# Kernel tuning notes

Hardware: AMD Instinct MI355X
Metric: run time of the kernel (lower is better)

## Reference

```python
import jax, jax.numpy as jnp
import numpy as np

CLASS_NUM = 20
C_FEAT = 256
STRIDE = 16
ROI = 7
SCALE = 1.0 / 16.0
TOPK = 300
NMS_THR = 0.7
SCORE_THR = 0.5
SAMPLES = 2  # nearest samples per bin edge in roi_pool


def _conv(x, W, b, stride, padding):
    y = jax.lax.conv_general_dilated(x, W, (stride, stride), padding,
                                     dimension_numbers=('NCHW', 'OIHW', 'NCHW'))
    return y + b[None, :, None, None]


def _pairwise_iou(boxes):
    x1, y1, x2, y2 = boxes[:, 0], boxes[:, 1], boxes[:, 2], boxes[:, 3]
    area = jnp.maximum(x2 - x1, 0.) * jnp.maximum(y2 - y1, 0.)
    ix1 = jnp.maximum(x1[:, None], x1[None, :])
    iy1 = jnp.maximum(y1[:, None], y1[None, :])
    ix2 = jnp.minimum(x2[:, None], x2[None, :])
    iy2 = jnp.minimum(y2[:, None], y2[None, :])
    inter = jnp.maximum(ix2 - ix1, 0.) * jnp.maximum(iy2 - iy1, 0.)
    return inter / jnp.maximum(area[:, None] + area[None, :] - inter, 1e-6)


def _nms(boxes, scores, valid, thr):
    # fixed-size greedy NMS: returns boolean keep mask aligned with input order
    K = boxes.shape[0]
    order = jnp.argsort(-scores)
    b = boxes[order]
    v = valid[order]
    iou = _pairwise_iou(b)  # [K,K]
    idx = jnp.arange(K)

    def body(i, keep):
        k = keep[i] & v[i]
        suppress = (iou[i] > thr) & (idx > i) & k
        return keep & (~suppress)

    keep = jax.lax.fori_loop(0, K, body, v)
    return jnp.zeros((K,), bool).at[order].set(keep)


def _roi_pool(f, boxes):
    # f: [C,H,W] feature map; boxes: [K,4] in image coords.
    # Max pool over ROI x SAMPLES nearest-neighbor samples per bin (jit-safe roi_pool).
    C, H, W = f.shape
    K = boxes.shape[0]
    b = boxes * SCALE
    frac = (jnp.arange(ROI)[:, None] + (jnp.arange(SAMPLES)[None, :] + 0.5) / SAMPLES).reshape(-1) / ROI
    xs = b[:, 0:1] + frac[None, :] * (b[:, 2:3] - b[:, 0:1])  # [K, ROI*S]
    ys = b[:, 1:2] + frac[None, :] * (b[:, 3:4] - b[:, 1:2])
    ix = jnp.clip(jnp.floor(xs), 0, W - 1).astype(jnp.int32)
    iy = jnp.clip(jnp.floor(ys), 0, H - 1).astype(jnp.int32)
    g = f[:, iy[:, :, None], ix[:, None, :]]  # [C,K,ROI*S,ROI*S]
    g = g.reshape(C, K, ROI, SAMPLES, ROI, SAMPLES)
    return g.max(axis=(3, 5)).transpose(1, 0, 2, 3)  # [K,C,ROI,ROI]


def setup_inputs() -> dict:
    key = jax.random.key(0)
    ks = jax.random.split(key, 12)
    img = 800
    x = jax.random.uniform(ks[0], (1, 3, img, img), jnp.float32)
    gt_boxes = jax.random.uniform(ks[1], (8, 5), jnp.float32) * img

    def w_(k, shape, fan_in):
        return jax.random.normal(k, shape, jnp.float32) * (1.0 / np.sqrt(fan_in))

    d_flat = ROI * ROI * C_FEAT
    return {
        'x': x, 'gt_boxes': gt_boxes,
        'W_feat': w_(ks[2], (C_FEAT, 3, STRIDE, STRIDE), 3 * STRIDE * STRIDE),
        'b_feat': jnp.zeros((C_FEAT,), jnp.float32),
        'W1': w_(ks[3], (C_FEAT, C_FEAT, 3, 3), C_FEAT * 9),
        'b1': jnp.zeros((C_FEAT,), jnp.float32),
        'Wc': w_(ks[4], (2, C_FEAT), C_FEAT),
        'bc': jnp.zeros((2,), jnp.float32),
        'Wb': w_(ks[5], (4, C_FEAT), C_FEAT),
        'bb': jnp.zeros((4,), jnp.float32),
        'fc1_w': w_(ks[6], (4096, d_flat), d_flat),
        'fc1_b': jnp.zeros((4096,), jnp.float32),
        'fc2_w': w_(ks[7], (4096, 4096), 4096),
        'fc2_b': jnp.zeros((4096,), jnp.float32),
        'cls_w': w_(ks[8], (CLASS_NUM + 1, 4096), 4096),
        'cls_b': jnp.zeros((CLASS_NUM + 1,), jnp.float32),
        'box_w': w_(ks[9], (4, 4096), 4096),
        'box_b': jnp.zeros((4,), jnp.float32),
        'w': 800, 'h': 800,
    }


def reference(x, gt_boxes, W_feat, b_feat, W1, b1, Wc, bc, Wb, bb,
              fc1_w, fc1_b, fc2_w, fc2_b, cls_w, cls_b, box_w, box_b, w, h):
    feature = _conv(x, W_feat, b_feat, STRIDE, 'VALID')          # [1,C,50,50]
    hmap = jax.nn.relu(_conv(feature, W1, b1, 1, 'SAME'))
    pre_labels = (jnp.einsum('nchw,oc->nhwo', hmap, Wc) + bc).reshape(-1, 2)
    pre_boxes = (jnp.einsum('nchw,oc->nhwo', hmap, Wb) + bb).reshape(-1, 4)
    logits = jax.nn.softmax(pre_labels, axis=-1)[:, 1]           # [2500]
    scores, idx = jax.lax.top_k(logits, TOPK)                    # fixed-size stand-in for score>thr select
    valid = scores > SCORE_THR
    pb = pre_boxes[idx]
    wf = jnp.float32(w)
    hf = jnp.float32(h)
    # box decode exactly as the original per-box loop (vectorized)
    x1 = jnp.maximum(pb[:, 2] - pb[:, 0] / 2, 0.)
    y1 = jnp.maximum(pb[:, 3] - pb[:, 1] / 2, 0.)
    x2 = jnp.minimum(pb[:, 2] + pb[:, 0], wf)
    y2 = jnp.minimum(pb[:, 3] + pb[:, 1], hf)
    boxes = jnp.stack([x1, y1, x2, y2], axis=-1)                 # [K,4]
    keep = _nms(boxes, scores, valid, NMS_THR)
    pooled = _roi_pool(feature[0], boxes)                        # [K,C,7,7]
    flat = pooled.reshape(TOPK, -1)
    h1 = jax.nn.relu(flat @ fc1_w.T + fc1_b)
    h2 = jax.nn.relu(h1 @ fc2_w.T + fc2_b)
    cls = h2 @ cls_w.T + cls_b                                   # [K,21]
    box = h2 @ box_w.T + box_b                                   # [K,4]
    out = jnp.where(keep[:, None], jnp.concatenate([cls, box], axis=-1), 0.)
    return out                                                   # [K,25]
```

## Files before the change

kernel.cpp:

```cpp
#include <hip/hip_runtime.h>
#include <hip/hip_bf16.h>
#include <math.h>

#define NPIX   2500
#define CFEAT  256
#define NTOP   300
#define DFLAT  12544
#define FCN    4096
#define FPSTRIDE 3328
#define KG1    392
#define KG2    128
#define MT     20

typedef _Float16 f16x8 __attribute__((ext_vector_type(8)));
typedef float    f32x4 __attribute__((ext_vector_type(4)));

static constexpr size_t OFF_FPAD  = 0;
static constexpr size_t OFF_SCORE = 0x5C0000;
static constexpr size_t OFF_PREB  = 0x5D0000;
static constexpr size_t OFF_KEEP  = 0x5E5000;
static constexpr size_t OFF_IX    = 0x5E6000;
static constexpr size_t OFF_IY    = 0x5EB000;
static constexpr size_t OFF_AFRAG = 0x600000;
static constexpr size_t OFF_H1F   = 0xE00000;
static constexpr size_t OFF_H2    = 0x1100000;
static constexpr size_t OFF_W1T   = 0x1600000;
static constexpr size_t OFF_PART  = 0x1900000;

__device__ inline float decode_dim(const void* p) {
    int iv = *(const int*)p;
    if (iv > 0 && iv < (1 << 20)) return (float)iv;
    return __int_as_float(iv);
}

__global__ void zero_fpad(float* __restrict__ fpad) {
    int i = blockIdx.x * 256 + threadIdx.x;
    if (i < 212992) *(float4*)(fpad + (size_t)i * 4) = make_float4(0.f, 0.f, 0.f, 0.f);
}

__global__ void __launch_bounds__(256)
patch_conv(const float* __restrict__ x, const float* __restrict__ Wf,
           const float* __restrict__ bf, float* __restrict__ fpad) {
    __shared__ float w[3072];
    int co0 = blockIdx.y * 4;
    for (int t = threadIdx.x; t < 3072; t += 256) w[t] = Wf[co0 * 768 + t];
    __syncthreads();
    int p = blockIdx.x * 256 + threadIdx.x;
    if (p >= NPIX) return;
    int py = p / 50, px = p % 50;
    float acc[4];
    #pragma unroll
    for (int c = 0; c < 4; ++c) acc[c] = bf[co0 + c];
    for (int ci = 0; ci < 3; ++ci) {
        const float* xp = x + ci * 640000 + (py * 16) * 800 + px * 16;
        #pragma unroll
        for (int ky = 0; ky < 16; ++ky) {
            const float* row = xp + ky * 800;
            #pragma unroll
            for (int kq = 0; kq < 4; ++kq) {
                float4 xv = *reinterpret_cast<const float4*>(row + kq * 4);
                int kb = ci * 256 + ky * 16 + kq * 4;
                #pragma unroll
                for (int c = 0; c < 4; ++c) {
                    const float* wc = w + c * 768 + kb;
                    acc[c] += xv.x * wc[0] + xv.y * wc[1] + xv.z * wc[2] + xv.w * wc[3];
                }
            }
        }
    }
    size_t o = (size_t)(py + 1) * 64 + (px + 1);
    #pragma unroll
    for (int c = 0; c < 4; ++c) fpad[(size_t)(co0 + c) * FPSTRIDE + o] = acc[c];
}

__global__ void transpose_w1(const float* __restrict__ W1, float* __restrict__ W1t) {
    int idx = blockIdx.x * 256 + threadIdx.x;
    if (idx >= 2304 * 256) return;
    int r = idx >> 8, co = idx & 255;
    W1t[idx] = W1[co * 2304 + r];
}

__global__ void __launch_bounds__(256)
conv3x3_part(const float* __restrict__ fpad, const float* __restrict__ W1t,
             float* __restrict__ cpart, int zci) {
    int co = threadIdx.x;
    int xb = blockIdx.x * 8;
    int y  = blockIdx.y;
    int z  = blockIdx.z;
    float acc[8];
    #pragma unroll
    for (int p = 0; p < 8; ++p) acc[p] = 0.0f;
    const float* fp = fpad + (size_t)(z * zci) * FPSTRIDE + (size_t)y * 64 + xb;
    const float* wp = W1t + (size_t)(z * zci) * 9 * 256 + co;
    #pragma unroll 2
    for (int ci = 0; ci < zci; ++ci) {
        float v[3][12];
        #pragma unroll
        for (int dy = 0; dy < 3; ++dy) {
            #pragma unroll
            for (int q = 0; q < 3; ++q) {
                float4 r4 = *(const float4*)(fp + dy * 64 + q * 4);
                v[dy][q * 4 + 0] = r4.x; v[dy][q * 4 + 1] = r4.y;
                v[dy][q * 4 + 2] = r4.z; v[dy][q * 4 + 3] = r4.w;
            }
        }
        float wv[9];
        #pragma unroll
        for (int k = 0; k < 9; ++k) wv[k] = wp[k * 256];
        #pragma unroll
        for (int dy = 0; dy < 3; ++dy)
            #pragma unroll
            for (int dx = 0; dx < 3; ++dx) {
                float wvv = wv[dy * 3 + dx];
                #pragma unroll
                for (int p = 0; p < 8; ++p)
                    acc[p] += v[dy][p + dx] * wvv;
            }
        fp += FPSTRIDE;
        wp += 9 * 256;
    }
    size_t base = (size_t)z * (NPIX * 256) + (size_t)(y * 50 + xb) * 256 + co;
    #pragma unroll
    for (int p = 0; p < 8; ++p)
        if (xb + p < 50) cpart[base + (size_t)p * 256] = acc[p];
}

__global__ void __launch_bounds__(256)
reducehead_k(const float* __restrict__ cpart, const float* __restrict__ b1,
             const float* __restrict__ Wc, const float* __restrict__ bc,
             const float* __restrict__ Wb, const float* __restrict__ bb,
             float* __restrict__ score, float* __restrict__ preb, int zs) {
    int lane = threadIdx.x & 63;
    int p = blockIdx.x * 4 + (threadIdx.x >> 6);
    if (p >= NPIX) return;
    size_t off = (size_t)p * 256 + lane * 4;
    float4 h = *(const float4*)(cpart + off);
    for (int z = 1; z < zs; ++z) {
        float4 v = *(const float4*)(cpart + (size_t)z * (NPIX * 256) + off);
        h.x += v.x; h.y += v.y; h.z += v.z; h.w += v.w;
    }
    float4 b = *(const float4*)(b1 + lane * 4);
    h.x = fmaxf(h.x + b.x, 0.f); h.y = fmaxf(h.y + b.y, 0.f);
    h.z = fmaxf(h.z + b.z, 0.f); h.w = fmaxf(h.w + b.w, 0.f);
    float4 c0 = *(const float4*)(Wc + lane * 4);
    float4 c1 = *(const float4*)(Wc + 256 + lane * 4);
    float4 w0 = *(const float4*)(Wb + lane * 4);
    float4 w1 = *(const float4*)(Wb + 256 + lane * 4);
    float4 w2 = *(const float4*)(Wb + 512 + lane * 4);
    float4 w3 = *(const float4*)(Wb + 768 + lane * 4);
    float s[6];
    s[0] = h.x*c0.x + h.y*c0.y + h.z*c0.z + h.w*c0.w;
    s[1] = h.x*c1.x + h.y*c1.y + h.z*c1.z + h.w*c1.w;
    s[2] = h.x*w0.x + h.y*w0.y + h.z*w0.z + h.w*w0.w;
    s[3] = h.x*w1.x + h.y*w1.y + h.z*w1.z + h.w*w1.w;
    s[4] = h.x*w2.x + h.y*w2.y + h.z*w2.z + h.w*w2.w;
    s[5] = h.x*w3.x + h.y*w3.y + h.z*w3.z + h.w*w3.w;
    #pragma unroll
    for (int o = 1; o < 64; o <<= 1) {
        #pragma unroll
        for (int q = 0; q < 6; ++q) s[q] += __shfl_xor(s[q], o, 64);
    }
    if (lane == 0) {
        float s0 = s[0] + bc[0], s1 = s[1] + bc[1];
        float m = fmaxf(s0, s1);
        float e0 = expf(s0 - m), e1 = expf(s1 - m);
        score[p] = e1 / (e0 + e1);
        preb[p * 4 + 0] = s[2] + bb[0];
        preb[p * 4 + 1] = s[3] + bb[1];
        preb[p * 4 + 2] = s[4] + bb[2];
        preb[p * 4 + 3] = s[5] + bb[3];
    }
}

__global__ void __launch_bounds__(1024)
topknms_k(const float* __restrict__ score, const float* __restrict__ preb,
          const void* wp_, const void* hp_, int* __restrict__ keep,
          int* __restrict__ ixb, int* __restrict__ iyb) {
    __shared__ float sv[4096];
    __shared__ int   si[4096];
    __shared__ float X1[320], Y1[320], X2[320], Y2[320], AR[320];
    __shared__ unsigned long long MASK[320][5];
    __shared__ unsigned long long KEEPW[5];
    int tid = threadIdx.x;
    int lane = tid & 63;
    int w = tid >> 6;

    for (int t = tid; t < 4096; t += 1024) {
        sv[t] = (t < NPIX) ? score[t] : -INFINITY;
        si[t] = t;
    }
    __syncthreads();
    for (int k = 2; k <= 4096; k <<= 1) {
        for (int j = k >> 1; j > 0; j >>= 1) {
            for (int t = tid; t < 4096; t += 1024) {
                int l = t ^ j;
                if (l > t) {
                    float vt = sv[t], vl = sv[l];
                    int it = si[t], il = si[l];
                    bool l_before_t = (vl > vt) || (vl == vt && il < it);
                    bool dir = ((t & k) == 0);
                    if (dir == l_before_t) {
                        sv[t] = vl; sv[l] = vt;
                        si[t] = il; si[l] = it;
                    }
                }
            }
            __syncthreads();
        }
    }

    if (tid < 320) {
        float x1 = 0.f, y1 = 0.f, x2 = 0.f, y2 = 0.f;
        bool v = false;
        if (tid < NTOP) {
            float wf = decode_dim(wp_), hf = decode_dim(hp_);
            int id = si[tid];
            float p0 = preb[id * 4 + 0], p1 = preb[id * 4 + 1];
            float p2 = preb[id * 4 + 2], p3 = preb[id * 4 + 3];
            x1 = fmaxf(p2 - p0 * 0.5f, 0.0f);
            y1 = fmaxf(p3 - p1 * 0.5f, 0.0f);
            x2 = fminf(p2 + p0, wf);
            y2 = fminf(p3 + p1, hf);
            v = sv[tid] > 0.5f;
            float bx1 = x1 * 0.0625f, by1 = y1 * 0.0625f;
            float bx2 = x2 * 0.0625f, by2 = y2 * 0.0625f;
            #pragma unroll
            for (int m = 0; m < 14; ++m) {
                int i = m >> 1, s = m & 1;
                float frac = ((float)i + (s ? 0.75f : 0.25f)) / 7.0f;
                float xs = bx1 + frac * (bx2 - bx1);
                float ys = by1 + frac * (by2 - by1);
                float fx = floorf(xs); fx = fminf(fmaxf(fx, 0.0f), 49.0f);
                float fy = floorf(ys); fy = fminf(fmaxf(fy, 0.0f), 49.0f);
                ixb[tid * 14 + m] = (int)fx;
                iyb[tid * 14 + m] = (int)fy;
            }
        }
        X1[tid] = x1; Y1[tid] = y1; X2[tid] = x2; Y2[tid] = y2;
        AR[tid] = fmaxf(x2 - x1, 0.0f) * fmaxf(y2 - y1, 0.0f);
        unsigned long long vb = __ballot(v);
        if (lane == 0) KEEPW[w] = vb;
    }
    __syncthreads();

    if (tid < 320) {
        float xi1 = X1[tid], yi1 = Y1[tid], xi2 = X2[tid], yi2 = Y2[tid], ai = AR[tid];
        #pragma unroll
        for (int jw = 0; jw < 5; ++jw) {
            unsigned long long mword = 0ull;
            #pragma unroll 4
            for (int j2 = 0; j2 < 64; ++j2) {
                int j = jw * 64 + j2;
                float ix1 = fmaxf(xi1, X1[j]);
                float iy1 = fmaxf(yi1, Y1[j]);
                float ix2 = fminf(xi2, X2[j]);
                float iy2 = fminf(yi2, Y2[j]);
                float inter = fmaxf(ix2 - ix1, 0.0f) * fmaxf(iy2 - iy1, 0.0f);
                float iou = inter / fmaxf(ai + AR[j] - inter, 1e-6f);
                bool sup = (iou > 0.7f) && (j > tid) && (j < NTOP);
                mword |= sup ? (1ull << j2) : 0ull;
            }
            MASK[tid][jw] = mword;
        }
    }
    __syncthreads();

    if (tid < 64) {
        unsigned long long m[5][5];
        #pragma unroll
        for (int g = 0; g < 5; ++g)
            #pragma unroll
            for (int q = 0; q < 5; ++q)
                m[g][q] = MASK[g * 64 + lane][q];
        unsigned long long kw0 = KEEPW[0], kw1 = KEEPW[1], kw2 = KEEPW[2],
                           kw3 = KEEPW[3], kw4 = KEEPW[4];
        #pragma unroll
        for (int g = 0; g < 5; ++g) {
            for (int i2 = 0; i2 < 64; ++i2) {
                unsigned long long kg = (g == 0) ? kw0 : (g == 1) ? kw1 :
                                        (g == 2) ? kw2 : (g == 3) ? kw3 : kw4;
                bool alive = (kg >> i2) & 1ull;
                unsigned long long b0 = __shfl(m[g][0], i2, 64);
                unsigned long long b1 = __shfl(m[g][1], i2, 64);
                unsigned long long b2 = __shfl(m[g][2], i2, 64);
                unsigned long long b3 = __shfl(m[g][3], i2, 64);
                unsigned long long b4 = __shfl(m[g][4], i2, 64);
                if (alive) {
                    kw0 &= ~b0; kw1 &= ~b1; kw2 &= ~b2; kw3 &= ~b3; kw4 &= ~b4;
                }
            }
        }
        #pragma unroll
        for (int g = 0; g < 5; ++g) {
            unsigned long long kg = (g == 0) ? kw0 : (g == 1) ? kw1 :
                                    (g == 2) ? kw2 : (g == 3) ? kw3 : kw4;
            int j = g * 64 + lane;
            if (j < NTOP) keep[j] = (int)((kg >> lane) & 1ull);
        }
    }
}

__global__ void __launch_bounds__(256)
roipool_frag(const float* __restrict__ fpad, const int* __restrict__ ixb,
             const int* __restrict__ iyb, _Float16* __restrict__ Af) {
    int wid = blockIdx.x * 256 + threadIdx.x;
    if (wid >= MT * KG1 * 64) return;
    int l = wid & 63;
    int g = (wid >> 6) % KG1;
    int T = wid / (KG1 * 64);
    int mm = T * 16 + (l & 15);
    int kbase = g * 32 + ((l >> 4) & 3) * 8;
    union { _Float16 h[8]; uint4 u; } o;
    if (mm < NTOP) {
        const int* ix = ixb + mm * 14;
        const int* iy = iyb + mm * 14;
        #pragma unroll
        for (int e = 0; e < 8; ++e) {
            int k = kbase + e;
            int c = k / 49, ij = k % 49, i = ij / 7, jx = ij % 7;
            int y0 = iy[2 * i] + 1, y1 = iy[2 * i + 1] + 1;
            int x0 = ix[2 * jx] + 1, x1 = ix[2 * jx + 1] + 1;
            const float* f = fpad + (size_t)c * FPSTRIDE;
            float v = fmaxf(fmaxf(f[y0 * 64 + x0], f[y0 * 64 + x1]),
                            fmaxf(f[y1 * 64 + x0], f[y1 * 64 + x1]));
            o.h[e] = (_Float16)v;
        }
    } else {
        o.u.x = 0u; o.u.y = 0u; o.u.z = 0u; o.u.w = 0u;
    }
    *(uint4*)(Af + (size_t)wid * 8) = o.u;
}

__global__ void __launch_bounds__(512)
gemm_fullm(const _Float16* __restrict__ Af, const float* __restrict__ B,
           float* __restrict__ part, int K, int KG, int kchunk) {
    __shared__ char Bs[2][64 * 128];
    int tid = threadIdx.x;
    int lane = tid & 63;
    int w = tid >> 6;
    int wm = w & 3, wn = w >> 2;
    int n0 = blockIdx.x * 64;
    int ks = blockIdx.y * kchunk;
    int nt = kchunk >> 6;

    f32x4 acc[5][2];
    #pragma unroll
    for (int tm = 0; tm < 5; ++tm)
        #pragma unroll
        for (int tn = 0; tn < 2; ++tn)
            acc[tm][tn] = f32x4{0.f, 0.f, 0.f, 0.f};

    int srow = tid >> 3;
    int skp  = (tid & 7) * 8;
    const float* bsrc = B + (size_t)(n0 + srow) * K + ks + skp;
    int sboff = srow * 128 + ((skp * 2) ^ ((srow & 7) << 4));

    float4 v0 = *(const float4*)(bsrc);
    float4 v1 = *(const float4*)(bsrc + 4);
    {
        union { _Float16 h[8]; uint4 u; } cv;
        cv.h[0] = (_Float16)v0.x; cv.h[1] = (_Float16)v0.y;
        cv.h[2] = (_Float16)v0.z; cv.h[3] = (_Float16)v0.w;
        cv.h[4] = (_Float16)v1.x; cv.h[5] = (_Float16)v1.y;
        cv.h[6] = (_Float16)v1.z; cv.h[7] = (_Float16)v1.w;
        *(uint4*)(Bs[0] + sboff) = cv.u;
    }
    if (nt > 1) {
        v0 = *(const float4*)(bsrc + 64);
        v1 = *(const float4*)(bsrc + 68);
    }
    __syncthreads();

    for (int k0 = 0; k0 < nt; ++k0) {
        const char* cur = Bs[k0 & 1];
        if (k0 + 1 < nt) {
            union { _Float16 h[8]; uint4 u; } cv;
            cv.h[0] = (_Float16)v0.x; cv.h[1] = (_Float16)v0.y;
            cv.h[2] = (_Float16)v0.z; cv.h[3] = (_Float16)v0.w;
            cv.h[4] = (_Float16)v1.x; cv.h[5] = (_Float16)v1.y;
            cv.h[6] = (_Float16)v1.z; cv.h[7] = (_Float16)v1.w;
            *(uint4*)(Bs[(k0 + 1) & 1] + sboff) = cv.u;
            if (k0 + 2 < nt) {
                v0 = *(const float4*)(bsrc + (k0 + 2) * 64);
                v1 = *(const float4*)(bsrc + (k0 + 2) * 64 + 4);
            }
        }
        #pragma unroll
        for (int kk = 0; kk < 2; ++kk) {
            int g = (ks + k0 * 64 + kk * 32) >> 5;
            f16x8 bfr[2];
            #pragma unroll
            for (int tn = 0; tn < 2; ++tn) {
                int row = wn * 32 + tn * 16 + (lane & 15);
                int kb = kk * 64 + (lane >> 4) * 16;
                bfr[tn] = *(const f16x8*)(cur + row * 128 + (kb ^ ((row & 7) << 4)));
            }
            #pragma unroll
            for (int tm = 0; tm < 5; ++tm) {
                int T = wm * 5 + tm;
                f16x8 a = *(const f16x8*)(Af + ((size_t)(T * KG + g) * 64 + lane) * 8);
                #pragma unroll
                for (int tn = 0; tn < 2; ++tn)
                    acc[tm][tn] = __builtin_amdgcn_mfma_f32_16x16x32_f16(a, bfr[tn], acc[tm][tn], 0, 0, 0);
            }
        }
        __syncthreads();
    }
    float* pout = part + (size_t)blockIdx.y * (NTOP * FCN);
    #pragma unroll
    for (int tm = 0; tm < 5; ++tm) {
        int mbase = (wm * 5 + tm) * 16 + (lane >> 4) * 4;
        #pragma unroll
        for (int j = 0; j < 4; ++j) {
            int m = mbase + j;
            if (m < NTOP) {
                #pragma unroll
                for (int tn = 0; tn < 2; ++tn) {
                    int n = n0 + wn * 32 + tn * 16 + (lane & 15);
                    pout[(size_t)m * FCN + n] = acc[tm][tn][j];
                }
            }
        }
    }
}

__global__ void reduce_fc1(const float* __restrict__ part, const float* __restrict__ bias,
                           _Float16* __restrict__ h1f, int ns) {
    int i = blockIdx.x * 256 + threadIdx.x;
    if (i >= NTOP * 512) return;
    int m = i >> 9;
    int f = (i & 511) * 8;
    float s[8];
    const float* p0 = part + (size_t)m * FCN + f;
    #pragma unroll
    for (int e = 0; e < 8; ++e) s[e] = p0[e];
    for (int z = 1; z < ns; ++z) {
        const float* pz = p0 + (size_t)z * (NTOP * FCN);
        #pragma unroll
        for (int e = 0; e < 8; ++e) s[e] += pz[e];
    }
    union { _Float16 h[8]; uint4 u; } o;
    #pragma unroll
    for (int e = 0; e < 8; ++e) o.h[e] = (_Float16)fmaxf(s[e] + bias[f + e], 0.0f);
    int T = m >> 4, g = f >> 5, l = (m & 15) + 16 * ((f >> 3) & 3);
    *(uint4*)(h1f + ((size_t)(T * KG2 + g) * 64 + l) * 8) = o.u;
}

__global__ void reduce_fc2(const float* __restrict__ part, const float* __restrict__ bias,
                           float* __restrict__ outp, int ns) {
    size_t i = (size_t)blockIdx.x * 256 + threadIdx.x;
    size_t mn4 = (size_t)NTOP * FCN / 4;
    if (i >= mn4) return;
    float4 s = *(const float4*)(part + i * 4);
    for (int zz = 1; zz < ns; ++zz) {
        float4 v = *(const float4*)(part + (size_t)zz * (NTOP * FCN) + i * 4);
        s.x += v.x; s.y += v.y; s.z += v.z; s.w += v.w;
    }
    int n = (int)((i * 4) % FCN);
    float4 b = *(const float4*)(bias + n);
    s.x = fmaxf(s.x + b.x, 0.f); s.y = fmaxf(s.y + b.y, 0.f);
    s.z = fmaxf(s.z + b.z, 0.f); s.w = fmaxf(s.w + b.w, 0.f);
    *(float4*)(outp + i * 4) = s;
}

__global__ void __launch_bounds__(256)
final_k(const float* __restrict__ h2, const float* __restrict__ clsw,
        const float* __restrict__ clsb, const float* __restrict__ boxw,
        const float* __restrict__ boxb, const int* __restrict__ keep,
        float* __restrict__ out) {
    int gid = blockIdx.x * 4 + (threadIdx.x >> 6);
    if (gid >= NTOP * 25) return;
    int lane = threadIdx.x & 63;
    int k = gid / 25, o = gid % 25;
    const float* w;
    float b;
    if (o < 21) { w = clsw + (size_t)o * 4096; b = clsb[o]; }
    else        { w = boxw + (size_t)(o - 21) * 4096; b = boxb[o - 21]; }
    const float* h = h2 + (size_t)k * 4096;
    float s = 0.0f;
    #pragma unroll
    for (int i = 0; i < 16; ++i) {
        float4 hv = *(const float4*)(h + (i * 64 + lane) * 4);
        float4 wv = *(const float4*)(w + (i * 64 + lane) * 4);
        s += hv.x * wv.x + hv.y * wv.y + hv.z * wv.z + hv.w * wv.w;
    }
    #pragma unroll
    for (int off = 1; off < 64; off <<= 1) s += __shfl_xor(s, off, 64);
    if (lane == 0) out[gid] = keep[k] ? (s + b) : 0.0f;
}

extern "C" void kernel_launch(void* const* d_in, const int* in_sizes, int n_in,
                              void* d_out, int out_size, void* d_ws, size_t ws_size,
                              hipStream_t stream) {
    const float* x    = (const float*)d_in[0];
    const float* Wf   = (const float*)d_in[2];
    const float* bf   = (const float*)d_in[3];
    const float* W1   = (const float*)d_in[4];
    const float* b1   = (const float*)d_in[5];
    const float* Wc   = (const float*)d_in[6];
    const float* bc   = (const float*)d_in[7];
    const float* Wb   = (const float*)d_in[8];
    const float* bb   = (const float*)d_in[9];
    const float* fc1w = (const float*)d_in[10];
    const float* fc1b = (const float*)d_in[11];
    const float* fc2w = (const float*)d_in[12];
    const float* fc2b = (const float*)d_in[13];
    const float* clsw = (const float*)d_in[14];
    const float* clsb = (const float*)d_in[15];
    const float* boxw = (const float*)d_in[16];
    const float* boxb = (const float*)d_in[17];
    const void*  wp   = d_in[18];
    const void*  hp   = d_in[19];

    char* ws = (char*)d_ws;
    float*     fpad  = (float*)(ws + OFF_FPAD);
    float*     score = (float*)(ws + OFF_SCORE);
    float*     preb  = (float*)(ws + OFF_PREB);
    int*       keep  = (int*)(ws + OFF_KEEP);
    int*       ixb   = (int*)(ws + OFF_IX);
    int*       iyb   = (int*)(ws + OFF_IY);
    _Float16*  Af    = (_Float16*)(ws + OFF_AFRAG);
    _Float16*  h1f   = (_Float16*)(ws + OFF_H1F);
    float*     h2    = (float*)(ws + OFF_H2);
    float*     w1t   = (float*)(ws + OFF_W1T);
    float*     out   = (float*)d_out;

    size_t slot = (size_t)NTOP * FCN * 4;
    size_t avail = ws_size > OFF_PART ? (ws_size - OFF_PART) / slot : 0;
    int ns1 = (avail >= 7) ? 7 : (avail >= 4) ? 4 : (avail >= 2) ? 2 : 1;
    int ns2 = (avail >= 4) ? 4 : (avail >= 2) ? 2 : 1;
    float* part1 = (avail >= 1) ? (float*)(ws + OFF_PART) : h2;
    float* part2 = (avail >= 1) ? (float*)(ws + OFF_PART) : (float*)Af;
    int kch1 = (196 / ns1) * 64;
    int kch2 = (64 / ns2) * 64;
    int zs = (avail >= 5) ? 8 : 4;
    float* cpart = (avail >= 5) ? (float*)(ws + OFF_PART) : (float*)(ws + OFF_AFRAG);

    zero_fpad<<<832, 256, 0, stream>>>(fpad);
    patch_conv<<<dim3(10, 64), 256, 0, stream>>>(x, Wf, bf, fpad);
    transpose_w1<<<(2304 * 256 + 255) / 256, 256, 0, stream>>>(W1, w1t);
    conv3x3_part<<<dim3(7, 50, zs), 256, 0, stream>>>(fpad, w1t, cpart, 256 / zs);
    reducehead_k<<<625, 256, 0, stream>>>(cpart, b1, Wc, bc, Wb, bb, score, preb, zs);
    topknms_k<<<1, 1024, 0, stream>>>(score, preb, wp, hp, keep, ixb, iyb);
    roipool_frag<<<(MT * KG1 * 64 + 255) / 256, 256, 0, stream>>>(fpad, ixb, iyb, Af);
    gemm_fullm<<<dim3(64, ns1), 512, 0, stream>>>(Af, fc1w, part1, DFLAT, KG1, kch1);
    reduce_fc1<<<(NTOP * 512 + 255) / 256, 256, 0, stream>>>(part1, fc1b, h1f, ns1);
    gemm_fullm<<<dim3(64, ns2), 512, 0, stream>>>(h1f, fc2w, part2, FCN, KG2, kch2);
    reduce_fc2<<<(NTOP * FCN / 4 + 255) / 256, 256, 0, stream>>>(part2, fc2b, h2, ns2);
    final_k<<<(NTOP * 25 + 3) / 4, 256, 0, stream>>>(h2, clsw, clsb, boxw, boxb, keep, out);
}
```

Before: 408.1 us.

## Replace bitonic sort with radix-select top-k and rank sort

Replaces the full 4096-element bitonic sort in the top-k/NMS kernel with an 8-pass radix select over packed (score, inverted index) 64-bit keys. The selected 300 keys are then ordered with an O(K^2) rank sort. This removes the many syncthreads-separated bitonic stages, at the cost of shared-memory atomics in each histogram pass. Score bit patterns are compared as unsigned integers, which orders correctly only for non-negative floats; softmax outputs meet that condition.

Measured after the change: 357.8 us. 1.14x faster.

```diff
diff --git a/kernel.cpp b/kernel.cpp
--- a/kernel.cpp
+++ b/kernel.cpp
@@ -176,8 +176,11 @@
 topknms_k(const float* __restrict__ score, const float* __restrict__ preb,
           const void* wp_, const void* hp_, int* __restrict__ keep,
           int* __restrict__ ixb, int* __restrict__ iyb) {
-    __shared__ float sv[4096];
-    __shared__ int   si[4096];
+    __shared__ unsigned long long KEYS[NPIX];
+    __shared__ unsigned int hist[256];
+    __shared__ int sh_digit, sh_newr, cnt;
+    __shared__ unsigned long long SEL[NTOP];
+    __shared__ unsigned long long SORT[NTOP];
     __shared__ float X1[320], Y1[320], X2[320], Y2[320], AR[320];
     __shared__ unsigned long long MASK[320][5];
     __shared__ unsigned long long KEEPW[5];
@@ -185,43 +188,88 @@
     int lane = tid & 63;
     int w = tid >> 6;
 
-    for (int t = tid; t < 4096; t += 1024) {
-        sv[t] = (t < NPIX) ? score[t] : -INFINITY;
-        si[t] = t;
-    }
-    __syncthreads();
-    for (int k = 2; k <= 4096; k <<= 1) {
-        for (int j = k >> 1; j > 0; j >>= 1) {
-            for (int t = tid; t < 4096; t += 1024) {
-                int l = t ^ j;
-                if (l > t) {
-                    float vt = sv[t], vl = sv[l];
-                    int it = si[t], il = si[l];
-                    bool l_before_t = (vl > vt) || (vl == vt && il < it);
-                    bool dir = ((t & k) == 0);
-                    if (dir == l_before_t) {
-                        sv[t] = vl; sv[l] = vt;
-                        si[t] = il; si[l] = it;
-                    }
+    for (int e = tid; e < NPIX; e += 1024) {
+        unsigned sb = __float_as_uint(score[e]);
+        KEYS[e] = ((unsigned long long)sb << 32) | (unsigned)(~e);
+    }
+    if (tid == 0) cnt = 0;
+    __syncthreads();
+
+    unsigned long long P = 0ull, M = 0ull;
+    int r = NTOP;
+    for (int pass = 0; pass < 8; ++pass) {
+        int shift = 56 - 8 * pass;
+        if (tid < 256) hist[tid] = 0u;
+        __syncthreads();
+        for (int e = tid; e < NPIX; e += 1024) {
+            unsigned long long k = KEYS[e];
+            if ((k & M) == P)
+                atomicAdd(&hist[(unsigned)(k >> shift) & 255u], 1u);
+        }
+        __syncthreads();
+        if (tid < 64) {
+            unsigned c0 = hist[tid * 4 + 0], c1 = hist[tid * 4 + 1];
+            unsigned c2 = hist[tid * 4 + 2], c3 = hist[tid * 4 + 3];
+            unsigned sl = c0 + c1 + c2 + c3;
+            unsigned suf = sl;
+            #pragma unroll
+            for (int off = 1; off < 64; off <<= 1) {
+                unsigned o = __shfl_down(suf, off, 64);
+                if (lane + off < 64) suf += o;
+            }
+            unsigned G = suf - sl;
+            if (G < (unsigned)r && G + sl >= (unsigned)r) {
+                unsigned above = G;
+                unsigned cc[4] = {c0, c1, c2, c3};
+                int d = 0; unsigned ab = above;
+                #pragma unroll
+                for (int i = 3; i >= 0; --i) {
+                    if (ab < (unsigned)r && ab + cc[i] >= (unsigned)r) { d = tid * 4 + i; break; }
+                    ab += cc[i];
                 }
-            }
-            __syncthreads();
-        }
-    }
+                sh_digit = d;
+                sh_newr = r - (int)ab;
+            }
+        }
+        __syncthreads();
+        P |= ((unsigned long long)(unsigned)sh_digit) << shift;
+        M |= 0xFFull << shift;
+        r = sh_newr;
+    }
+    unsigned long long T = P;
+
+    for (int e = tid; e < NPIX; e += 1024) {
+        unsigned long long k = KEYS[e];
+        if (k >= T) {
+            int s = atomicAdd(&cnt, 1);
+            SEL[s] = k;
+        }
+    }
+    __syncthreads();
+
+    if (tid < NTOP) {
+        unsigned long long mine = SEL[tid];
+        int rank = 0;
+        for (int j = 0; j < NTOP; ++j) rank += (SEL[j] > mine) ? 1 : 0;
+        SORT[rank] = mine;
+    }
+    __syncthreads();
 
     if (tid < 320) {
         float x1 = 0.f, y1 = 0.f, x2 = 0.f, y2 = 0.f;
         bool v = false;
         if (tid < NTOP) {
+            unsigned long long key = SORT[tid];
+            int id = (int)(~(unsigned)key);
+            float sc = __uint_as_float((unsigned)(key >> 32));
             float wf = decode_dim(wp_), hf = decode_dim(hp_);
-            int id = si[tid];
             float p0 = preb[id * 4 + 0], p1 = preb[id * 4 + 1];
             float p2 = preb[id * 4 + 2], p3 = preb[id * 4 + 3];
             x1 = fmaxf(p2 - p0 * 0.5f, 0.0f);
             y1 = fmaxf(p3 - p1 * 0.5f, 0.0f);
             x2 = fminf(p2 + p0, wf);
             y2 = fminf(p3 + p1, hf);
-            v = sv[tid] > 0.5f;
+            v = sc > 0.5f;
             float bx1 = x1 * 0.0625f, by1 = y1 * 0.0625f;
             float bx2 = x2 * 0.0625f, by2 = y2 * 0.0625f;
             #pragma unroll
@@ -239,7 +287,7 @@
         X1[tid] = x1; Y1[tid] = y1; X2[tid] = x2; Y2[tid] = y2;
         AR[tid] = fmaxf(x2 - x1, 0.0f) * fmaxf(y2 - y1, 0.0f);
         unsigned long long vb = __ballot(v);
-        if (lane == 0) KEEPW[w] = vb;
+        if (lane == 0 && w < 5) KEEPW[w] = vb;
     }
     __syncthreads();
 
```
